# Performance work log

Hardware: AMD Instinct MI355X
Metric: run time of the kernel (lower is better)

The kernel has to match this reference:

```python
import jax, jax.numpy as jnp
import numpy as np

N_NODES = 100000
N_EDGES = 500000
D = 128


def setup_inputs() -> dict:
    key = jax.random.key(0)
    ks = jax.random.split(key, 6)
    x = jax.random.normal(ks[0], (N_NODES, D), dtype=jnp.float32)
    edge_index = jax.random.randint(ks[1], (2, N_EDGES), 0, N_NODES, dtype=jnp.int64)
    edge_label = jax.random.randint(ks[2], (N_EDGES,), 0, 2, dtype=jnp.int64)
    # MLP params (dim_in -> dim_in, 2 layers, has_act=True, has_bias=True)
    scale = 1.0 / np.sqrt(D)
    W1 = jax.random.normal(ks[3], (D, D), dtype=jnp.float32) * scale
    b1 = jnp.zeros((D,), dtype=jnp.float32)
    W2 = jax.random.normal(ks[4], (D, D), dtype=jnp.float32) * scale
    b2 = jnp.zeros((D,), dtype=jnp.float32)
    return {"x": x, "edge_index": edge_index, "edge_label": edge_label,
            "W1": W1, "b1": b1, "W2": W2, "b2": b2}


def reference(x, edge_index, edge_label, W1, b1, W2, b2):
    # post-MP MLP on all node features (has_act=True -> ReLU after each layer)
    h = jax.nn.relu(x @ W1 + b1)          # [N, D]
    h = jax.nn.relu(h @ W2 + b2)          # [N, D]
    # gather endpoints: batch.x[edge_index] -> [2, E, D]
    v1 = h[edge_index[0]]                  # [E, D]
    v2 = h[edge_index[1]]                  # [E, D]
    # dot decode: sum(v1 * v2, dim=-1)
    pred = jnp.sum(v1 * v2, axis=-1)       # [E]
    return pred, edge_label
```

## Files before the change

### kernel.cpp

```cpp
#include <hip/hip_runtime.h>
#include <hip/hip_bf16.h>

typedef __attribute__((ext_vector_type(8))) short short8;
typedef __attribute__((ext_vector_type(4))) float floatx4;

#define DFEAT 128
#define PITCH 136
#define ROWS_PER_BLOCK 64

__device__ __forceinline__ unsigned short f2bf(float f) {
  unsigned u = __float_as_uint(f);
  u += 0x7FFFu + ((u >> 16) & 1u);
  return (unsigned short)(u >> 16);
}

__global__ __launch_bounds__(256) void mlp2_kernel(
    const float* __restrict__ x, const float* __restrict__ W1,
    const float* __restrict__ b1, const float* __restrict__ W2,
    const float* __restrict__ b2, unsigned short* __restrict__ h2,
    int nNodes) {
  __shared__ unsigned short sW[DFEAT * PITCH];
  __shared__ unsigned short sH[ROWS_PER_BLOCK * PITCH];

  const int tid = threadIdx.x;
  const int wave = tid >> 6;
  const int lane = tid & 63;
  const int quad = lane >> 4;
  const int l16 = lane & 15;
  const int rowbase = blockIdx.x * ROWS_PER_BLOCK + wave * 16;

  #pragma unroll 4
  for (int i = 0; i < 64; ++i) {
    int e = i * 256 + tid;
    int k = e >> 7, n = e & 127;
    sW[n * PITCH + k] = f2bf(W1[e]);
  }
  __syncthreads();

  floatx4 acc[8];
  #pragma unroll
  for (int n0 = 0; n0 < 8; ++n0) acc[n0] = (floatx4){0.f, 0.f, 0.f, 0.f};

  const int m = rowbase + l16;
  const bool mvalid = (m < nNodes);

  #pragma unroll
  for (int kk = 0; kk < 4; ++kk) {
    const int kbase = kk * 32 + quad * 8;
    short8 a;
    if (mvalid) {
      const float* xp = x + (size_t)m * DFEAT + kbase;
      float4 f0 = *(const float4*)(xp);
      float4 f1 = *(const float4*)(xp + 4);
      a[0] = (short)f2bf(f0.x); a[1] = (short)f2bf(f0.y);
      a[2] = (short)f2bf(f0.z); a[3] = (short)f2bf(f0.w);
      a[4] = (short)f2bf(f1.x); a[5] = (short)f2bf(f1.y);
      a[6] = (short)f2bf(f1.z); a[7] = (short)f2bf(f1.w);
    } else {
      a = (short8){0,0,0,0,0,0,0,0};
    }
    #pragma unroll
    for (int n0 = 0; n0 < 8; ++n0) {
      short8 b = *(const short8*)&sW[(n0 * 16 + l16) * PITCH + kbase];
      acc[n0] = __builtin_amdgcn_mfma_f32_16x16x32_bf16(a, b, acc[n0], 0, 0, 0);
    }
  }

  #pragma unroll
  for (int n0 = 0; n0 < 8; ++n0) {
    int col = n0 * 16 + l16;
    float bias = b1[col];
    #pragma unroll
    for (int r = 0; r < 4; ++r) {
      float v = acc[n0][r] + bias;
      v = v > 0.f ? v : 0.f;
      int rl = wave * 16 + quad * 4 + r;
      sH[rl * PITCH + col] = f2bf(v);
    }
  }
  __syncthreads();

  #pragma unroll 4
  for (int i = 0; i < 64; ++i) {
    int e = i * 256 + tid;
    int k = e >> 7, n = e & 127;
    sW[n * PITCH + k] = f2bf(W2[e]);
  }
  __syncthreads();

  #pragma unroll
  for (int n0 = 0; n0 < 8; ++n0) acc[n0] = (floatx4){0.f, 0.f, 0.f, 0.f};

  #pragma unroll
  for (int kk = 0; kk < 4; ++kk) {
    const int kbase = kk * 32 + quad * 8;
    short8 a = *(const short8*)&sH[(wave * 16 + l16) * PITCH + kbase];
    #pragma unroll
    for (int n0 = 0; n0 < 8; ++n0) {
      short8 b = *(const short8*)&sW[(n0 * 16 + l16) * PITCH + kbase];
      acc[n0] = __builtin_amdgcn_mfma_f32_16x16x32_bf16(a, b, acc[n0], 0, 0, 0);
    }
  }

  #pragma unroll
  for (int n0 = 0; n0 < 8; ++n0) {
    int col = n0 * 16 + l16;
    float bias = b2[col];
    #pragma unroll
    for (int r = 0; r < 4; ++r) {
      float v = acc[n0][r] + bias;
      v = v > 0.f ? v : 0.f;
      int g = rowbase + quad * 4 + r;
      if (g < nNodes) h2[(size_t)g * DFEAT + col] = f2bf(v);
    }
  }
}

__device__ __forceinline__ float dot2bf(unsigned a, unsigned b, float acc) {
  float a0 = __uint_as_float(a << 16);
  float a1 = __uint_as_float(a & 0xFFFF0000u);
  float b0 = __uint_as_float(b << 16);
  float b1 = __uint_as_float(b & 0xFFFF0000u);
  acc = fmaf(a0, b0, acc);
  acc = fmaf(a1, b1, acc);
  return acc;
}

__global__ __launch_bounds__(256) void edge_kernel(
    const unsigned short* __restrict__ h2, const int* __restrict__ eidx,
    const int* __restrict__ elabel, float* __restrict__ out, int E) {
  const int sub = threadIdx.x & 15;
  const int e = blockIdx.x * 16 + (threadIdx.x >> 4);
  if (e < E) {
    int s = eidx[e];
    int d = eidx[E + e];
    const uint4 ua = *(const uint4*)(h2 + (size_t)s * DFEAT + sub * 8);
    const uint4 ub = *(const uint4*)(h2 + (size_t)d * DFEAT + sub * 8);
    float acc = 0.f;
    acc = dot2bf(ua.x, ub.x, acc);
    acc = dot2bf(ua.y, ub.y, acc);
    acc = dot2bf(ua.z, ub.z, acc);
    acc = dot2bf(ua.w, ub.w, acc);
    acc += __shfl_xor(acc, 8);
    acc += __shfl_xor(acc, 4);
    acc += __shfl_xor(acc, 2);
    acc += __shfl_xor(acc, 1);
    if (sub == 0) out[e] = acc;
  }
  if (threadIdx.x < 16) {
    int le = blockIdx.x * 16 + threadIdx.x;
    if (le < E) out[E + le] = (float)elabel[le];
  }
}

extern "C" void kernel_launch(void* const* d_in, const int* in_sizes, int n_in,
                              void* d_out, int out_size, void* d_ws, size_t ws_size,
                              hipStream_t stream) {
  const float* x  = (const float*)d_in[0];
  const int* eidx = (const int*)d_in[1];
  const int* elab = (const int*)d_in[2];
  const float* W1 = (const float*)d_in[3];
  const float* b1 = (const float*)d_in[4];
  const float* W2 = (const float*)d_in[5];
  const float* b2 = (const float*)d_in[6];
  float* out = (float*)d_out;

  const int nNodes = in_sizes[0] / DFEAT;
  const int E = in_sizes[2];

  unsigned short* h2 = (unsigned short*)d_ws;

  const int mlpBlocks = (nNodes + ROWS_PER_BLOCK - 1) / ROWS_PER_BLOCK;
  mlp2_kernel<<<mlpBlocks, 256, 0, stream>>>(x, W1, b1, W2, b2, h2, nNodes);

  const int edgeBlocks = (E + 15) / 16;
  edge_kernel<<<edgeBlocks, 256, 0, stream>>>(h2, eidx, elab, out, E);
}
```

Baseline: 166.5 us.

## Split MLP into persistent per-layer kernels with swizzled LDS and batched edge gathers

The fused two-layer MLP kernel is split into two persistent kernels over a fixed grid of 512 blocks. Each block stages its weight matrix into LDS once, using coalesced loads and an XOR swizzle in place of padding, then loops over 16-row tiles per wave. Outputs are restaged through LDS so global stores are full 16-byte rows. Layer 2 reads the bf16 intermediate back from global memory in place, which adds a round trip of traffic. The edge kernel now handles four edges per 16-lane group, keeping more gathers in flight, and writes labels with a grid-stride loop.

```diff
diff --git a/kernel.cpp b/kernel.cpp
--- a/kernel.cpp
+++ b/kernel.cpp
@@ -1,12 +1,12 @@
 #include <hip/hip_runtime.h>
-#include <hip/hip_bf16.h>
 
 typedef __attribute__((ext_vector_type(8))) short short8;
+typedef __attribute__((ext_vector_type(4))) short short4v;
 typedef __attribute__((ext_vector_type(4))) float floatx4;
 
-#define DFEAT 128
-#define PITCH 136
-#define ROWS_PER_BLOCK 64
+#define D 128
+#define NWAVES 4
+#define GRID_MLP 512
 
 __device__ __forceinline__ unsigned short f2bf(float f) {
   unsigned u = __float_as_uint(f);
@@ -14,104 +14,153 @@
   return (unsigned short)(u >> 16);
 }
 
-__global__ __launch_bounds__(256) void mlp2_kernel(
+__device__ __forceinline__ void stageW(const float* __restrict__ W,
+                                       unsigned short* __restrict__ sW, int tid) {
+  const int n = tid & 127;
+  const int tg = tid >> 7;
+  #pragma unroll
+  for (int iter = 0; iter < 16; ++iter) {
+    const int k0 = iter * 8 + tg * 4;
+    float w0 = W[(k0 + 0) * D + n];
+    float w1 = W[(k0 + 1) * D + n];
+    float w2 = W[(k0 + 2) * D + n];
+    float w3 = W[(k0 + 3) * D + n];
+    short4v p;
+    p[0] = (short)f2bf(w0); p[1] = (short)f2bf(w1);
+    p[2] = (short)f2bf(w2); p[3] = (short)f2bf(w3);
+    const int idx = n * D + (((k0 >> 3) ^ (n & 15)) << 3) + (k0 & 7);
+    *(short4v*)&sW[idx] = p;
+  }
+}
+
+
+__global__ __launch_bounds__(256) void mlp_layer1(
     const float* __restrict__ x, const float* __restrict__ W1,
-    const float* __restrict__ b1, const float* __restrict__ W2,
-    const float* __restrict__ b2, unsigned short* __restrict__ h2,
-    int nNodes) {
-  __shared__ unsigned short sW[DFEAT * PITCH];
-  __shared__ unsigned short sH[ROWS_PER_BLOCK * PITCH];
-
+    const float* __restrict__ b1, unsigned short* __restrict__ h,
+    int nNodes, int ntiles) {
+  __shared__ unsigned short sW[D * D];
+  __shared__ unsigned short sH[NWAVES][16 * D];
   const int tid = threadIdx.x;
-  const int wave = tid >> 6;
-  const int lane = tid & 63;
-  const int quad = lane >> 4;
-  const int l16 = lane & 15;
-  const int rowbase = blockIdx.x * ROWS_PER_BLOCK + wave * 16;
-
-  #pragma unroll 4
-  for (int i = 0; i < 64; ++i) {
-    int e = i * 256 + tid;
-    int k = e >> 7, n = e & 127;
-    sW[n * PITCH + k] = f2bf(W1[e]);
-  }
+  const int wave = tid >> 6, lane = tid & 63;
+  const int quad = lane >> 4, l16 = lane & 15;
+
+  stageW(W1, sW, tid);
   __syncthreads();
 
-  floatx4 acc[8];
-  #pragma unroll
-  for (int n0 = 0; n0 < 8; ++n0) acc[n0] = (floatx4){0.f, 0.f, 0.f, 0.f};
-
-  const int m = rowbase + l16;
-  const bool mvalid = (m < nNodes);
-
-  #pragma unroll
-  for (int kk = 0; kk < 4; ++kk) {
-    const int kbase = kk * 32 + quad * 8;
-    short8 a;
-    if (mvalid) {
-      const float* xp = x + (size_t)m * DFEAT + kbase;
-      float4 f0 = *(const float4*)(xp);
-      float4 f1 = *(const float4*)(xp + 4);
+  float bias[8];
+  #pragma unroll
+  for (int n0 = 0; n0 < 8; ++n0) bias[n0] = b1[n0 * 16 + l16];
+
+  unsigned short* mysH = sH[wave];
+
+  for (int t = blockIdx.x * NWAVES + wave; t < ntiles; t += GRID_MLP * NWAVES) {
+    const int m = t * 16 + l16;
+    const bool mv = (m < nNodes);
+    float4 xf[8];
+    const float* xp = x + (size_t)m * D + quad * 8;
+    #pragma unroll
+    for (int kk = 0; kk < 4; ++kk) {
+      if (mv) {
+        xf[2 * kk]     = *(const float4*)(xp + kk * 32);
+        xf[2 * kk + 1] = *(const float4*)(xp + kk * 32 + 4);
+      } else {
+        xf[2 * kk] = make_float4(0, 0, 0, 0);
+        xf[2 * kk + 1] = make_float4(0, 0, 0, 0);
+      }
+    }
+    floatx4 acc[8];
+    #pragma unroll
+    for (int n0 = 0; n0 < 8; ++n0) acc[n0] = (floatx4){0.f, 0.f, 0.f, 0.f};
+    #pragma unroll
+    for (int kk = 0; kk < 4; ++kk) {
+      const float4 f0 = xf[2 * kk], f1 = xf[2 * kk + 1];
+      short8 a;
       a[0] = (short)f2bf(f0.x); a[1] = (short)f2bf(f0.y);
       a[2] = (short)f2bf(f0.z); a[3] = (short)f2bf(f0.w);
       a[4] = (short)f2bf(f1.x); a[5] = (short)f2bf(f1.y);
       a[6] = (short)f2bf(f1.z); a[7] = (short)f2bf(f1.w);
-    } else {
-      a = (short8){0,0,0,0,0,0,0,0};
+      #pragma unroll
+      for (int n0 = 0; n0 < 8; ++n0) {
+        short8 b = *(const short8*)&sW[(n0 * 16 + l16) * D + (((kk * 4 + quad) ^ l16) << 3)];
+        acc[n0] = __builtin_amdgcn_mfma_f32_16x16x32_bf16(a, b, acc[n0], 0, 0, 0);
+      }
     }
     #pragma unroll
     for (int n0 = 0; n0 < 8; ++n0) {
-      short8 b = *(const short8*)&sW[(n0 * 16 + l16) * PITCH + kbase];
-      acc[n0] = __builtin_amdgcn_mfma_f32_16x16x32_bf16(a, b, acc[n0], 0, 0, 0);
-    }
-  }
-
-  #pragma unroll
-  for (int n0 = 0; n0 < 8; ++n0) {
-    int col = n0 * 16 + l16;
-    float bias = b1[col];
-    #pragma unroll
-    for (int r = 0; r < 4; ++r) {
-      float v = acc[n0][r] + bias;
-      v = v > 0.f ? v : 0.f;
-      int rl = wave * 16 + quad * 4 + r;
-      sH[rl * PITCH + col] = f2bf(v);
-    }
-  }
+      #pragma unroll
+      for (int r = 0; r < 4; ++r) {
+        float v = acc[n0][r] + bias[n0];
+        v = v > 0.f ? v : 0.f;
+        const int row = quad * 4 + r;
+        const int g = 2 * n0 + (l16 >> 3);
+        mysH[row * D + (((g ^ row) & 15) << 3) + (l16 & 7)] = f2bf(v);
+      }
+    }
+    #pragma unroll
+    for (int i = 0; i < 4; ++i) {
+      const int row = i * 4 + quad;
+      short8 vrow = *(const short8*)&mysH[row * D + (((l16 ^ row) & 15) << 3)];
+      const int g = t * 16 + row;
+      if (g < nNodes) *(short8*)&h[(size_t)g * D + l16 * 8] = vrow;
+    }
+  }
+}
+
+__global__ __launch_bounds__(256) void mlp_layer2(
+    unsigned short* __restrict__ h, const float* __restrict__ W2,
+    const float* __restrict__ b2, int nNodes, int ntiles) {
+  __shared__ unsigned short sW[D * D];
+  __shared__ unsigned short sH[NWAVES][16 * D];
+  const int tid = threadIdx.x;
+  const int wave = tid >> 6, lane = tid & 63;
+  const int quad = lane >> 4, l16 = lane & 15;
+
+  stageW(W2, sW, tid);
   __syncthreads();
 
-  #pragma unroll 4
-  for (int i = 0; i < 64; ++i) {
-    int e = i * 256 + tid;
-    int k = e >> 7, n = e & 127;
-    sW[n * PITCH + k] = f2bf(W2[e]);
-  }
-  __syncthreads();
-
-  #pragma unroll
-  for (int n0 = 0; n0 < 8; ++n0) acc[n0] = (floatx4){0.f, 0.f, 0.f, 0.f};
-
-  #pragma unroll
-  for (int kk = 0; kk < 4; ++kk) {
-    const int kbase = kk * 32 + quad * 8;
-    short8 a = *(const short8*)&sH[(wave * 16 + l16) * PITCH + kbase];
+  float bias[8];
+  #pragma unroll
+  for (int n0 = 0; n0 < 8; ++n0) bias[n0] = b2[n0 * 16 + l16];
+
+  unsigned short* mysH = sH[wave];
+
+  for (int t = blockIdx.x * NWAVES + wave; t < ntiles; t += GRID_MLP * NWAVES) {
+    const int m = t * 16 + l16;
+    const bool mv = (m < nNodes);
+    short8 af[4];
+    #pragma unroll
+    for (int kk = 0; kk < 4; ++kk) {
+      if (mv) af[kk] = *(const short8*)&h[(size_t)m * D + kk * 32 + quad * 8];
+      else    af[kk] = (short8){0, 0, 0, 0, 0, 0, 0, 0};
+    }
+    floatx4 acc[8];
+    #pragma unroll
+    for (int n0 = 0; n0 < 8; ++n0) acc[n0] = (floatx4){0.f, 0.f, 0.f, 0.f};
+    #pragma unroll
+    for (int kk = 0; kk < 4; ++kk) {
+      #pragma unroll
+      for (int n0 = 0; n0 < 8; ++n0) {
+        short8 b = *(const short8*)&sW[(n0 * 16 + l16) * D + (((kk * 4 + quad) ^ l16) << 3)];
+        acc[n0] = __builtin_amdgcn_mfma_f32_16x16x32_bf16(af[kk], b, acc[n0], 0, 0, 0);
+      }
+    }
     #pragma unroll
     for (int n0 = 0; n0 < 8; ++n0) {
-      short8 b = *(const short8*)&sW[(n0 * 16 + l16) * PITCH + kbase];
-      acc[n0] = __builtin_amdgcn_mfma_f32_16x16x32_bf16(a, b, acc[n0], 0, 0, 0);
-    }
-  }
-
-  #pragma unroll
-  for (int n0 = 0; n0 < 8; ++n0) {
-    int col = n0 * 16 + l16;
-    float bias = b2[col];
-    #pragma unroll
-    for (int r = 0; r < 4; ++r) {
-      float v = acc[n0][r] + bias;
-      v = v > 0.f ? v : 0.f;
-      int g = rowbase + quad * 4 + r;
-      if (g < nNodes) h2[(size_t)g * DFEAT + col] = f2bf(v);
+      #pragma unroll
+      for (int r = 0; r < 4; ++r) {
+        float v = acc[n0][r] + bias[n0];
+        v = v > 0.f ? v : 0.f;
+        const int row = quad * 4 + r;
+        const int g = 2 * n0 + (l16 >> 3);
+        mysH[row * D + (((g ^ row) & 15) << 3) + (l16 & 7)] = f2bf(v);
+      }
+    }
+    #pragma unroll
+    for (int i = 0; i < 4; ++i) {
+      const int row = i * 4 + quad;
+      short8 vrow = *(const short8*)&mysH[row * D + (((l16 ^ row) & 15) << 3)];
+      const int g = t * 16 + row;
+      if (g < nNodes) *(short8*)&h[(size_t)g * D + l16 * 8] = vrow;
     }
   }
 }
@@ -130,27 +179,37 @@
     const unsigned short* __restrict__ h2, const int* __restrict__ eidx,
     const int* __restrict__ elabel, float* __restrict__ out, int E) {
   const int sub = threadIdx.x & 15;
-  const int e = blockIdx.x * 16 + (threadIdx.x >> 4);
-  if (e < E) {
-    int s = eidx[e];
-    int d = eidx[E + e];
-    const uint4 ua = *(const uint4*)(h2 + (size_t)s * DFEAT + sub * 8);
-    const uint4 ub = *(const uint4*)(h2 + (size_t)d * DFEAT + sub * 8);
-    float acc = 0.f;
-    acc = dot2bf(ua.x, ub.x, acc);
-    acc = dot2bf(ua.y, ub.y, acc);
-    acc = dot2bf(ua.z, ub.z, acc);
-    acc = dot2bf(ua.w, ub.w, acc);
-    acc += __shfl_xor(acc, 8);
-    acc += __shfl_xor(acc, 4);
-    acc += __shfl_xor(acc, 2);
-    acc += __shfl_xor(acc, 1);
-    if (sub == 0) out[e] = acc;
-  }
-  if (threadIdx.x < 16) {
-    int le = blockIdx.x * 16 + threadIdx.x;
-    if (le < E) out[E + le] = (float)elabel[le];
-  }
+  const int grp = (blockIdx.x * 256 + threadIdx.x) >> 4;
+  const int e0 = grp * 4;
+  uint4 va[4], vb[4];
+  #pragma unroll
+  for (int i = 0; i < 4; ++i) {
+    const int e = e0 + i;
+    if (e < E) {
+      const int s = eidx[e];
+      const int d = eidx[E + e];
+      va[i] = *(const uint4*)(h2 + (size_t)s * D + sub * 8);
+      vb[i] = *(const uint4*)(h2 + (size_t)d * D + sub * 8);
+    }
+  }
+  #pragma unroll
+  for (int i = 0; i < 4; ++i) {
+    const int e = e0 + i;
+    if (e < E) {
+      float acc = 0.f;
+      acc = dot2bf(va[i].x, vb[i].x, acc);
+      acc = dot2bf(va[i].y, vb[i].y, acc);
+      acc = dot2bf(va[i].z, vb[i].z, acc);
+      acc = dot2bf(va[i].w, vb[i].w, acc);
+      acc += __shfl_xor(acc, 8);
+      acc += __shfl_xor(acc, 4);
+      acc += __shfl_xor(acc, 2);
+      acc += __shfl_xor(acc, 1);
+      if (sub == 0) out[e] = acc;
+    }
+  }
+  for (int le = blockIdx.x * 256 + threadIdx.x; le < E; le += gridDim.x * 256)
+    out[E + le] = (float)elabel[le];
 }
 
 extern "C" void kernel_launch(void* const* d_in, const int* in_sizes, int n_in,
@@ -165,14 +224,15 @@
   const float* b2 = (const float*)d_in[6];
   float* out = (float*)d_out;
 
-  const int nNodes = in_sizes[0] / DFEAT;
+  const int nNodes = in_sizes[0] / D;
   const int E = in_sizes[2];
-
-  unsigned short* h2 = (unsigned short*)d_ws;
-
-  const int mlpBlocks = (nNodes + ROWS_PER_BLOCK - 1) / ROWS_PER_BLOCK;
-  mlp2_kernel<<<mlpBlocks, 256, 0, stream>>>(x, W1, b1, W2, b2, h2, nNodes);
-
-  const int edgeBlocks = (E + 15) / 16;
-  edge_kernel<<<edgeBlocks, 256, 0, stream>>>(h2, eidx, elab, out, E);
-}
+  const int ntiles = (nNodes + 15) / 16;
+
+  unsigned short* h = (unsigned short*)d_ws;
+
+  mlp_layer1<<<GRID_MLP, 256, 0, stream>>>(x, W1, b1, h, nNodes, ntiles);
+  mlp_layer2<<<GRID_MLP, 256, 0, stream>>>(h, W2, b2, nNodes, ntiles);
+
+  const int edgeBlocks = (E + 63) / 64;
+  edge_kernel<<<edgeBlocks, 256, 0, stream>>>(h, eidx, elab, out, E);
+}
```

New measurement: 147.6 us. -11.4%, faster.
